# Kernel optimization log

Measured on AMD Instinct MI355X. Metric: run time of the kernel, lower is better.

Reference implementation:

```python
import jax, jax.numpy as jnp
import numpy as np

EPS = 0.1    # entropic regularization for the approximate OT (auction-style) solve
ITERS = 20   # fixed number of Sinkhorn sweeps (mirrors fixed-iteration auction kernel)


def setup_inputs() -> dict:
    key = jax.random.key(0)
    k1, k2 = jax.random.split(key)
    pc_gen = jax.random.normal(k1, (2, 4096, 3), dtype=jnp.float32)
    pc_gt = jax.random.normal(k2, (2, 4096, 3), dtype=jnp.float32)
    return {"pc_gen": pc_gen, "pc_gt": pc_gt}


def _emd_loss(pc_gen, pc_gt):
    # Pairwise squared Euclidean cost: [B, N1, N2]
    C = jnp.sum((pc_gen[:, :, None, :] - pc_gt[:, None, :, :]) ** 2, axis=-1)
    B, N1, N2 = C.shape
    loga = -jnp.log(jnp.asarray(N1, C.dtype))  # uniform source marginal (log 1/N1)
    logb = -jnp.log(jnp.asarray(N2, C.dtype))  # uniform target marginal (log 1/N2)

    def step(carry, _):
        f, g = carry
        # log-domain Sinkhorn updates (numerically stable)
        f = EPS * (loga - jax.scipy.special.logsumexp((g[:, None, :] - C) / EPS, axis=2))
        g = EPS * (logb - jax.scipy.special.logsumexp((f[:, :, None] - C) / EPS, axis=1))
        return (f, g), None

    init = (jnp.zeros((B, N1), C.dtype), jnp.zeros((B, N2), C.dtype))
    (f, g), _ = jax.lax.scan(jax.checkpoint(step), init, None, length=ITERS)

    # Transport plan and expected matching cost per cloud.
    P = jnp.exp((f[:, :, None] + g[:, None, :] - C) / EPS)  # [B, N1, N2]
    per_cloud = jnp.sum(P * C, axis=(1, 2))  # equals (total match cost)/N1
    # Original: dist = sum of matched distances; emd_loss = (dist / N1).mean()
    return jnp.mean(per_cloud)


def reference(pc_gen, pc_gt):
    return _emd_loss(pc_gen, pc_gt)
```

## Files before the change

### kernel.cpp

```cpp
#include <hip/hip_runtime.h>


#define N   4096
#define NT  512
#define RPB 8
#define NW  (NT / 64)

constexpr float EPS_F  = 0.1f;
constexpr float SHIFT  = 60.0f;
constexpr float LOG_A  = -8.317766166719343f;
constexpr float C10L   = 14.426950408889634f;
constexpr float C20L   = 28.853900817779268f;
constexpr float SHIFTL = 86.56170245333781f;
constexpr float NLN2T  = -0.06931471805599453f;
constexpr float LN2    = 0.6931471805599453f;

extern "C" __device__ float __ocml_native_exp2_f32(float);

__device__ __forceinline__ float fast_exp2(float x) {
#if __has_builtin(__builtin_amdgcn_exp2f)
    return __builtin_amdgcn_exp2f(x);
#else
    return __ocml_native_exp2_f32(x);
#endif
}

__device__ __forceinline__ float rfl(float x) {
    return __int_as_float(__builtin_amdgcn_readfirstlane(__float_as_int(x)));
}

__global__ __launch_bounds__(256) void prep_kernel(
    const float* __restrict__ gen, const float* __restrict__ gt,
    float4* __restrict__ genPack, float4* __restrict__ gtPack,
    float* __restrict__ wBaseGen, float* __restrict__ wBaseGt,
    float* __restrict__ fg, float* __restrict__ out)
{
    int t = blockIdx.x * 256 + threadIdx.x;
    int cloud = t >> 13;
    int idx   = t & 8191;
    const float* src = cloud ? gt : gen;
    float x = src[idx * 3 + 0];
    float y = src[idx * 3 + 1];
    float z = src[idx * 3 + 2];
    float nb = -C10L * fmaf(z, z, fmaf(y, y, x * x));
    (cloud ? gtPack : genPack)[idx] = make_float4(x, y, z, SHIFTL + nb);
    (cloud ? wBaseGt : wBaseGen)[idx] = nb;
    fg[t] = 0.0f;
    if (t == 0) out[0] = 0.0f;
}

__global__ __launch_bounds__(NT, 8) void sweep_kernel(
    float4*       __restrict__ packRow,
    const float4* __restrict__ packCol,
    const float*  __restrict__ wBaseRow,
    float*        __restrict__ dualRaw)
{
    const int b   = blockIdx.y;
    const int tid = threadIdx.x;
    const int rowBase = blockIdx.x * RPB;

    float4*      rp = packRow  + (size_t)b * N + rowBase;
    const float* wb = wBaseRow + (size_t)b * N + rowBase;

    float X[RPB], Y[RPB], Z[RPB], S[RPB];
    #pragma unroll
    for (int r = 0; r < RPB; ++r) {
        float4 q = rp[r];
        X[r] = rfl(q.x * C20L);
        Y[r] = rfl(q.y * C20L);
        Z[r] = rfl(q.z * C20L);
        S[r] = rfl(wb[r]);
    }

    const float4* cp = packCol + (size_t)b * N;

    float acc[RPB];
    #pragma unroll
    for (int r = 0; r < RPB; ++r) acc[r] = 0.0f;

    #pragma unroll
    for (int k = 0; k < N / NT; ++k) {
        float4 p = cp[tid + NT * k];
        #pragma unroll
        for (int r = 0; r < RPB; ++r) {
            float t = fmaf(Z[r], p.z, p.w);
            t = fmaf(Y[r], p.y, t);
            t = fmaf(X[r], p.x, t);
            acc[r] += fast_exp2(t + S[r]);
        }
    }

    #pragma unroll
    for (int r = 0; r < RPB; ++r) {
        float a = acc[r];
        a += __shfl_xor(a, 32);
        a += __shfl_xor(a, 16);
        a += __shfl_xor(a, 8);
        a += __shfl_xor(a, 4);
        a += __shfl_xor(a, 2);
        a += __shfl_xor(a, 1);
        acc[r] = a;
    }
    __shared__ float sred[RPB][NW];
    const int wave = tid >> 6, lane = tid & 63;
    if (lane == 0) {
        #pragma unroll
        for (int r = 0; r < RPB; ++r) sred[r][wave] = acc[r];
    }
    __syncthreads();
    if (tid < RPB) {
        float s = 0.f;
        #pragma unroll
        for (int w = 0; w < NW; ++w) s += sred[tid][w];
        float dual = EPS_F * (LOG_A + SHIFT - log2f(s) * LN2);
        dualRaw[(size_t)b * N + rowBase + tid] = dual;
        ((float*)(rp + tid))[3] = fmaf(dual, C10L, SHIFTL + wb[tid]);
    }
}

__global__ __launch_bounds__(NT, 8) void loss_kernel(
    const float4* __restrict__ packGen,
    const float4* __restrict__ packGt,
    const float*  __restrict__ wBaseGen,
    const float*  __restrict__ f,
    const float*  __restrict__ g,
    float*        __restrict__ out)
{
    const int b   = blockIdx.y;
    const int tid = threadIdx.x;
    const int rowBase = blockIdx.x * RPB;

    const float4* rp = packGen  + (size_t)b * N + rowBase;
    const float*  wb = wBaseGen + (size_t)b * N + rowBase;
    const float*  fp = f        + (size_t)b * N + rowBase;

    float Ax[RPB], Ay[RPB], Az[RPB], Ri[RPB], F2[RPB];
    #pragma unroll
    for (int r = 0; r < RPB; ++r) {
        float4 q = rp[r];
        Ax[r] = rfl(q.x * -2.0f);
        Ay[r] = rfl(q.y * -2.0f);
        Az[r] = rfl(q.z * -2.0f);
        Ri[r] = rfl(wb[r] * NLN2T);
        F2[r] = rfl(fp[r] * C10L);
    }

    const float4* cp = packGt + (size_t)b * N;
    const float*  gc = g      + (size_t)b * N;

    float acc = 0.0f;
    #pragma unroll
    for (int k = 0; k < N / NT; ++k) {
        float4 p  = cp[tid + NT * k];
        float  gj = gc[tid + NT * k];
        float  G2 = gj * C10L;
        float  rj = fmaf(p.w - SHIFTL, NLN2T, gj);
        #pragma unroll
        for (int r = 0; r < RPB; ++r) {
            float cc = rj + Ri[r];
            cc = fmaf(Az[r], p.z, cc);
            cc = fmaf(Ay[r], p.y, cc);
            cc = fmaf(Ax[r], p.x, cc);
            float arg = fmaf(cc, -C10L, G2 + F2[r]);
            acc = fmaf(fast_exp2(arg), cc, acc);
        }
    }

    acc += __shfl_xor(acc, 32);
    acc += __shfl_xor(acc, 16);
    acc += __shfl_xor(acc, 8);
    acc += __shfl_xor(acc, 4);
    acc += __shfl_xor(acc, 2);
    acc += __shfl_xor(acc, 1);
    __shared__ float sred[NW];
    const int wave = tid >> 6, lane = tid & 63;
    if (lane == 0) sred[wave] = acc;
    __syncthreads();
    if (tid == 0) {
        float t = 0.f;
        #pragma unroll
        for (int w = 0; w < NW; ++w) t += sred[w];
        atomicAdd(out, t * 0.5f);
    }
}

extern "C" void kernel_launch(void* const* d_in, const int* in_sizes, int n_in,
                              void* d_out, int out_size, void* d_ws, size_t ws_size,
                              hipStream_t stream) {
    const float* gen = (const float*)d_in[0];
    const float* gt  = (const float*)d_in[1];
    float* out = (float*)d_out;

    char* ws = (char*)d_ws;
    float4* genPack  = (float4*)ws;
    float4* gtPack   = (float4*)(ws + 128 * 1024);
    float*  wBaseGen = (float*)(ws + 256 * 1024);
    float*  wBaseGt  = (float*)(ws + 288 * 1024);
    float*  f        = (float*)(ws + 320 * 1024);
    float*  g        = f + 2 * N;

    prep_kernel<<<dim3(16384 / 256), 256, 0, stream>>>(
        gen, gt, genPack, gtPack, wBaseGen, wBaseGt, f, out);

    const dim3 grid(N / RPB, 2);
    for (int it = 0; it < 20; ++it) {
        sweep_kernel<<<grid, NT, 0, stream>>>(genPack, gtPack, wBaseGen, f);
        sweep_kernel<<<grid, NT, 0, stream>>>(gtPack, genPack, wBaseGt, g);
    }
    loss_kernel<<<grid, NT, 0, stream>>>(genPack, gtPack, wBaseGen, f, g, out);
}
```

Before: 425.5 us.

## Fuse all Sinkhorn sweeps into one persistent kernel with grid barriers

```diff
diff --git a/kernel.cpp b/kernel.cpp
--- a/kernel.cpp
+++ b/kernel.cpp
@@ -1,10 +1,12 @@
 #include <hip/hip_runtime.h>
 
 
-#define N   4096
-#define NT  512
-#define RPB 8
-#define NW  (NT / 64)
+#define N    4096
+#define NT   512
+#define RPB  16
+#define NBLK 512
+#define NW   (NT / 64)
+#define KIT  (N / NT)
 
 constexpr float EPS_F  = 0.1f;
 constexpr float SHIFT  = 60.0f;
@@ -29,36 +31,45 @@
     return __int_as_float(__builtin_amdgcn_readfirstlane(__float_as_int(x)));
 }
 
-__global__ __launch_bounds__(256) void prep_kernel(
-    const float* __restrict__ gen, const float* __restrict__ gt,
-    float4* __restrict__ genPack, float4* __restrict__ gtPack,
-    float* __restrict__ wBaseGen, float* __restrict__ wBaseGt,
-    float* __restrict__ fg, float* __restrict__ out)
+struct alignas(128) PadU { unsigned int v; unsigned int pad[31]; };
+__device__ PadU g_bucket[32];
+__device__ PadU g_root;
+__device__ PadU g_epoch;
+
+__device__ __forceinline__ void grid_barrier(int blk) {
+    __syncthreads();
+    if (threadIdx.x == 0) {
+        __threadfence();
+        unsigned my = __hip_atomic_load(&g_epoch.v, __ATOMIC_RELAXED,
+                                        __HIP_MEMORY_SCOPE_AGENT);
+        int bucket = blk & 31;
+        unsigned old = __hip_atomic_fetch_add(&g_bucket[bucket].v, 1u,
+                                              __ATOMIC_ACQ_REL, __HIP_MEMORY_SCOPE_AGENT);
+        if (old == (NBLK / 32) - 1) {
+            __hip_atomic_store(&g_bucket[bucket].v, 0u, __ATOMIC_RELAXED,
+                               __HIP_MEMORY_SCOPE_AGENT);
+            unsigned r = __hip_atomic_fetch_add(&g_root.v, 1u,
+                                                __ATOMIC_ACQ_REL, __HIP_MEMORY_SCOPE_AGENT);
+            if (r == 31u) {
+                __hip_atomic_store(&g_root.v, 0u, __ATOMIC_RELAXED,
+                                   __HIP_MEMORY_SCOPE_AGENT);
+                __hip_atomic_fetch_add(&g_epoch.v, 1u, __ATOMIC_RELEASE,
+                                       __HIP_MEMORY_SCOPE_AGENT);
+            }
+        }
+        while (__hip_atomic_load(&g_epoch.v, __ATOMIC_RELAXED,
+                                 __HIP_MEMORY_SCOPE_AGENT) == my)
+            __builtin_amdgcn_s_sleep(2);
+        __threadfence();
+    }
+    __syncthreads();
+}
+
+__device__ __forceinline__ void half_sweep(
+    float4*       packRow, const float4* packCol,
+    const float*  wBaseRow, float* dualRaw,
+    int b, int rowBase, int tid)
 {
-    int t = blockIdx.x * 256 + threadIdx.x;
-    int cloud = t >> 13;
-    int idx   = t & 8191;
-    const float* src = cloud ? gt : gen;
-    float x = src[idx * 3 + 0];
-    float y = src[idx * 3 + 1];
-    float z = src[idx * 3 + 2];
-    float nb = -C10L * fmaf(z, z, fmaf(y, y, x * x));
-    (cloud ? gtPack : genPack)[idx] = make_float4(x, y, z, SHIFTL + nb);
-    (cloud ? wBaseGt : wBaseGen)[idx] = nb;
-    fg[t] = 0.0f;
-    if (t == 0) out[0] = 0.0f;
-}
-
-__global__ __launch_bounds__(NT, 8) void sweep_kernel(
-    float4*       __restrict__ packRow,
-    const float4* __restrict__ packCol,
-    const float*  __restrict__ wBaseRow,
-    float*        __restrict__ dualRaw)
-{
-    const int b   = blockIdx.y;
-    const int tid = threadIdx.x;
-    const int rowBase = blockIdx.x * RPB;
-
     float4*      rp = packRow  + (size_t)b * N + rowBase;
     const float* wb = wBaseRow + (size_t)b * N + rowBase;
 
@@ -79,7 +90,7 @@
     for (int r = 0; r < RPB; ++r) acc[r] = 0.0f;
 
     #pragma unroll
-    for (int k = 0; k < N / NT; ++k) {
+    for (int k = 0; k < KIT; ++k) {
         float4 p = cp[tid + NT * k];
         #pragma unroll
         for (int r = 0; r < RPB; ++r) {
@@ -118,69 +129,96 @@
     }
 }
 
-__global__ __launch_bounds__(NT, 8) void loss_kernel(
-    const float4* __restrict__ packGen,
-    const float4* __restrict__ packGt,
-    const float*  __restrict__ wBaseGen,
-    const float*  __restrict__ f,
-    const float*  __restrict__ g,
-    float*        __restrict__ out)
+__global__ __launch_bounds__(NT, 4) void fused_kernel(
+    const float* __restrict__ gen, const float* __restrict__ gt,
+    float4* __restrict__ genPack, float4* __restrict__ gtPack,
+    float* __restrict__ wBaseGen, float* __restrict__ wBaseGt,
+    float* __restrict__ f, float* __restrict__ g,
+    float* __restrict__ out)
 {
-    const int b   = blockIdx.y;
     const int tid = threadIdx.x;
-    const int rowBase = blockIdx.x * RPB;
-
-    const float4* rp = packGen  + (size_t)b * N + rowBase;
-    const float*  wb = wBaseGen + (size_t)b * N + rowBase;
-    const float*  fp = f        + (size_t)b * N + rowBase;
-
-    float Ax[RPB], Ay[RPB], Az[RPB], Ri[RPB], F2[RPB];
-    #pragma unroll
-    for (int r = 0; r < RPB; ++r) {
-        float4 q = rp[r];
-        Ax[r] = rfl(q.x * -2.0f);
-        Ay[r] = rfl(q.y * -2.0f);
-        Az[r] = rfl(q.z * -2.0f);
-        Ri[r] = rfl(wb[r] * NLN2T);
-        F2[r] = rfl(fp[r] * C10L);
-    }
-
-    const float4* cp = packGt + (size_t)b * N;
-    const float*  gc = g      + (size_t)b * N;
-
-    float acc = 0.0f;
-    #pragma unroll
-    for (int k = 0; k < N / NT; ++k) {
-        float4 p  = cp[tid + NT * k];
-        float  gj = gc[tid + NT * k];
-        float  G2 = gj * C10L;
-        float  rj = fmaf(p.w - SHIFTL, NLN2T, gj);
+    const int blk = blockIdx.x;
+    const int b   = blk >> 8;
+    const int rowBase = (blk & 255) * RPB;
+
+    {
+        int t = blk * NT + tid;
+        if (t < 16384) {
+            int cloud = t >> 13;
+            int idx   = t & 8191;
+            const float* src = cloud ? gt : gen;
+            float x = src[idx * 3 + 0];
+            float y = src[idx * 3 + 1];
+            float z = src[idx * 3 + 2];
+            float nb = -C10L * fmaf(z, z, fmaf(y, y, x * x));
+            (cloud ? gtPack : genPack)[idx] = make_float4(x, y, z, SHIFTL + nb);
+            (cloud ? wBaseGt : wBaseGen)[idx] = nb;
+            (cloud ? g : f)[idx] = 0.0f;
+            if (t == 0) out[0] = 0.0f;
+        }
+    }
+    grid_barrier(blk);
+
+    for (int it = 0; it < 20; ++it) {
+        half_sweep(genPack, gtPack, wBaseGen, f, b, rowBase, tid);
+        grid_barrier(blk);
+        half_sweep(gtPack, genPack, wBaseGt, g, b, rowBase, tid);
+        grid_barrier(blk);
+    }
+
+    {
+        const float4* rp = genPack  + (size_t)b * N + rowBase;
+        const float*  wb = wBaseGen + (size_t)b * N + rowBase;
+        const float*  fp = f        + (size_t)b * N + rowBase;
+
+        float Ax[RPB], Ay[RPB], Az[RPB], Ri[RPB], F2[RPB];
         #pragma unroll
         for (int r = 0; r < RPB; ++r) {
-            float cc = rj + Ri[r];
-            cc = fmaf(Az[r], p.z, cc);
-            cc = fmaf(Ay[r], p.y, cc);
-            cc = fmaf(Ax[r], p.x, cc);
-            float arg = fmaf(cc, -C10L, G2 + F2[r]);
-            acc = fmaf(fast_exp2(arg), cc, acc);
-        }
-    }
-
-    acc += __shfl_xor(acc, 32);
-    acc += __shfl_xor(acc, 16);
-    acc += __shfl_xor(acc, 8);
-    acc += __shfl_xor(acc, 4);
-    acc += __shfl_xor(acc, 2);
-    acc += __shfl_xor(acc, 1);
-    __shared__ float sred[NW];
-    const int wave = tid >> 6, lane = tid & 63;
-    if (lane == 0) sred[wave] = acc;
-    __syncthreads();
-    if (tid == 0) {
-        float t = 0.f;
-        #pragma unroll
-        for (int w = 0; w < NW; ++w) t += sred[w];
-        atomicAdd(out, t * 0.5f);
+            float4 q = rp[r];
+            Ax[r] = rfl(q.x * -2.0f);
+            Ay[r] = rfl(q.y * -2.0f);
+            Az[r] = rfl(q.z * -2.0f);
+            Ri[r] = rfl(wb[r] * NLN2T);
+            F2[r] = rfl(fp[r] * C10L);
+        }
+
+        const float4* cp = gtPack + (size_t)b * N;
+        const float*  gc = g      + (size_t)b * N;
+
+        float acc = 0.0f;
+        #pragma unroll
+        for (int k = 0; k < KIT; ++k) {
+            float4 p  = cp[tid + NT * k];
+            float  gj = gc[tid + NT * k];
+            float  G2 = gj * C10L;
+            float  rj = fmaf(p.w - SHIFTL, NLN2T, gj);
+            #pragma unroll
+            for (int r = 0; r < RPB; ++r) {
+                float cc = rj + Ri[r];
+                cc = fmaf(Az[r], p.z, cc);
+                cc = fmaf(Ay[r], p.y, cc);
+                cc = fmaf(Ax[r], p.x, cc);
+                float arg = fmaf(cc, -C10L, G2 + F2[r]);
+                acc = fmaf(fast_exp2(arg), cc, acc);
+            }
+        }
+
+        acc += __shfl_xor(acc, 32);
+        acc += __shfl_xor(acc, 16);
+        acc += __shfl_xor(acc, 8);
+        acc += __shfl_xor(acc, 4);
+        acc += __shfl_xor(acc, 2);
+        acc += __shfl_xor(acc, 1);
+        __shared__ float sredL[NW];
+        const int wave = tid >> 6, lane = tid & 63;
+        if (lane == 0) sredL[wave] = acc;
+        __syncthreads();
+        if (tid == 0) {
+            float t = 0.f;
+            #pragma unroll
+            for (int w = 0; w < NW; ++w) t += sredL[w];
+            atomicAdd(out, t * 0.5f);
+        }
     }
 }
 
@@ -199,13 +237,6 @@
     float*  f        = (float*)(ws + 320 * 1024);
     float*  g        = f + 2 * N;
 
-    prep_kernel<<<dim3(16384 / 256), 256, 0, stream>>>(
-        gen, gt, genPack, gtPack, wBaseGen, wBaseGt, f, out);
-
-    const dim3 grid(N / RPB, 2);
-    for (int it = 0; it < 20; ++it) {
-        sweep_kernel<<<grid, NT, 0, stream>>>(genPack, gtPack, wBaseGen, f);
-        sweep_kernel<<<grid, NT, 0, stream>>>(gtPack, genPack, wBaseGt, g);
-    }
-    loss_kernel<<<grid, NT, 0, stream>>>(genPack, gtPack, wBaseGen, f, g, out);
-}
+    fused_kernel<<<dim3(NBLK), dim3(NT), 0, stream>>>(
+        gen, gt, genPack, gtPack, wBaseGen, wBaseGt, f, g, out);
+}
```

Result: slower. 1.456 ms (+242.1%).
